# Kernel tuning notes

Hardware: AMD Instinct MI355X
Metric: run time of the kernel (lower is better)

Reference implementation:

```python
import jax, jax.numpy as jnp
import numpy as np

DIM = 1024
N_HEADS = 16
HEAD_DIM = DIM // N_HEADS
SCALE = HEAD_DIM ** -0.5


def setup_inputs() -> dict:
    key = jax.random.key(0)
    ks = jax.random.split(key, 5)
    B, N = 2, 2048
    x = jax.random.normal(ks[0], (B, N, DIM), dtype=jnp.float32)
    # torch Linear: y = x @ W.T + b, W shape (out, in)
    qkv_w = jax.random.normal(ks[1], (3 * DIM, DIM), dtype=jnp.float32) * (DIM ** -0.5)
    qkv_b = jax.random.normal(ks[2], (3 * DIM,), dtype=jnp.float32) * 0.02
    proj_w = jax.random.normal(ks[3], (DIM, DIM), dtype=jnp.float32) * (DIM ** -0.5)
    proj_b = jax.random.normal(ks[4], (DIM,), dtype=jnp.float32) * 0.02
    return {"x": x, "qkv_w": qkv_w, "qkv_b": qkv_b, "proj_w": proj_w, "proj_b": proj_b}


def reference(x, qkv_w, qkv_b, proj_w, proj_b):
    B, N, D = x.shape
    qkv = x @ qkv_w.T + qkv_b                      # [B, N, 3D]
    qkv = qkv.reshape(B, N, 3, N_HEADS, HEAD_DIM)
    qkv = jnp.transpose(qkv, (2, 0, 3, 1, 4))      # [3, B, H, N, hd]
    q, k, v = qkv[0], qkv[1], qkv[2]
    dp = jnp.einsum('bhqd,bhkd->bhqk', q, k) * SCALE  # [B, H, N, N]
    attn = jax.nn.softmax(dp, axis=-1)
    wa = jnp.einsum('bhqk,bhkd->bhqd', attn, v)    # [B, H, N, hd]
    wa = jnp.transpose(wa, (0, 2, 1, 3)).reshape(B, N, D)
    return wa @ proj_w.T + proj_b
```

## Files before the change

kernel.cpp:

```cpp
#include <hip/hip_runtime.h>

#define BATCH 2
#define SEQ   2048
#define DIM   1024
#define NHEAD 16
#define HD    64
#define BH    (BATCH * NHEAD)
#define SCALE 0.125f
#define LOG2E 1.44269504f
#define NTK   16

typedef __attribute__((ext_vector_type(8))) short short8;
typedef __attribute__((ext_vector_type(4))) short short4v;
typedef __attribute__((ext_vector_type(4))) float f32x4;
typedef __attribute__((ext_vector_type(16))) float f32x16;
typedef __attribute__((ext_vector_type(2))) unsigned int uint2v;

#define MFMA16(a, b, c) __builtin_amdgcn_mfma_f32_16x16x32_bf16(a, b, c, 0, 0, 0)
#define MFMA32(a, b, c) __builtin_amdgcn_mfma_f32_32x32x16_bf16(a, b, c, 0, 0, 0)

__device__ __forceinline__ ushort f2bf(float f) {
    union { float f; unsigned u; } v;
    v.f = f;
    unsigned r = (v.u + 0x7FFF + ((v.u >> 16) & 1)) >> 16;
    return (ushort)r;
}

__device__ __forceinline__ uint4 ld8f_bf16(const float* p) {
    float4 f0 = *(const float4*)p;
    float4 f1 = *(const float4*)(p + 4);
    union { ushort us[8]; uint4 v; } u;
    u.us[0] = f2bf(f0.x); u.us[1] = f2bf(f0.y);
    u.us[2] = f2bf(f0.z); u.us[3] = f2bf(f0.w);
    u.us[4] = f2bf(f1.x); u.us[5] = f2bf(f1.y);
    u.us[6] = f2bf(f1.z); u.us[7] = f2bf(f1.w);
    return u.v;
}

__device__ __forceinline__ void gl_lds16(const ushort* g, ushort* l) {
    __builtin_amdgcn_global_load_lds(
        (const __attribute__((address_space(1))) unsigned int*)g,
        (__attribute__((address_space(3))) unsigned int*)l,
        16, 0, 0);
}

__device__ __forceinline__ short8 ld_op(const ushort* base, int a1) {
    union { short4v h[2]; short8 v; } u;
    u.h[0] = *(const short4v*)&base[a1];
    u.h[1] = *(const short4v*)&base[a1 ^ 4];
    return u.v;
}

#define N_X  (BATCH * SEQ * DIM)
#define N_QW (3 * DIM * DIM)
#define N_PW (DIM * DIM)

__global__ __launch_bounds__(256) void cvt_kernel(
    const float* __restrict__ x, const float* __restrict__ qw,
    const float* __restrict__ pw, ushort* __restrict__ xb,
    ushort* __restrict__ qwb, ushort* __restrict__ pwb)
{
    const int i = (blockIdx.x * 256 + threadIdx.x) * 8;
    if (i < N_X)  *(uint4*)(xb  + i) = ld8f_bf16(x  + i);
    if (i < N_QW) *(uint4*)(qwb + i) = ld8f_bf16(qw + i);
    if (i < N_PW) *(uint4*)(pwb + i) = ld8f_bf16(pw + i);
}

template <int MODE, int WM, typename TOUT>
__global__ __launch_bounds__(256, 2) void gemm_bt(
    const ushort* __restrict__ A, const ushort* __restrict__ W,
    const float* __restrict__ bias, TOUT* __restrict__ out,
    int M, int Nout, int K)
{
    constexpr int BM = 2 * WM * 16;
    __shared__ __align__(16) ushort As[2][BM * 32];
    __shared__ __align__(16) ushort Bs[2][128 * 32];

    const int tid  = threadIdx.x;
    const int wave = tid >> 6, lane = tid & 63;
    const int quad = lane >> 4, l16 = lane & 15;
    const int wm = wave >> 1, wn = wave & 1;
    const int m0 = blockIdx.y * BM, n0 = blockIdx.x * 128;

    const int c0 = tid, c1 = tid + 256;
    const ushort* gA0 = A + (size_t)(m0 + (c0 >> 2)) * K + (c0 & 3) * 8;
    const ushort* gA1 = A + (size_t)(m0 + (c1 >> 2)) * K + (c1 & 3) * 8;
    const ushort* gB0 = W + (size_t)(n0 + (c0 >> 2)) * K + (c0 & 3) * 8;
    const ushort* gB1 = W + (size_t)(n0 + (c1 >> 2)) * K + (c1 & 3) * 8;

#define STAGE_G(buf, k0)                                                  \
    {                                                                     \
        gl_lds16(gA0 + (k0), &As[buf][(wave * 64) * 8]);                  \
        if (WM == 4) gl_lds16(gA1 + (k0), &As[buf][(wave * 64 + 256) * 8]); \
        gl_lds16(gB0 + (k0), &Bs[buf][(wave * 64) * 8]);                  \
        gl_lds16(gB1 + (k0), &Bs[buf][(wave * 64 + 256) * 8]);            \
    }

    f32x4 acc[WM][4];
#pragma unroll
    for (int i = 0; i < WM; i++)
#pragma unroll
        for (int j = 0; j < 4; j++) acc[i][j] = (f32x4){0.f, 0.f, 0.f, 0.f};

    const int KT = K >> 5;
    STAGE_G(0, 0)

    for (int kt = 0; kt < KT; kt++) {
        const int cur = kt & 1;
        __syncthreads();
        if (kt + 1 < KT) STAGE_G(cur ^ 1, (kt + 1) * 32)

        short8 af[WM], bfr[4];
#pragma unroll
        for (int mt = 0; mt < WM; mt++)
            af[mt] = *(const short8*)&As[cur][(wm * (WM * 16) + mt * 16 + l16) * 32 + quad * 8];
#pragma unroll
        for (int nt = 0; nt < 4; nt++)
            bfr[nt] = *(const short8*)&Bs[cur][(wn * 64 + nt * 16 + l16) * 32 + quad * 8];
#pragma unroll
        for (int mt = 0; mt < WM; mt++)
#pragma unroll
            for (int nt = 0; nt < 4; nt++)
                acc[mt][nt] = MFMA16(af[mt], bfr[nt], acc[mt][nt]);
    }

#pragma unroll
    for (int nt = 0; nt < 4; nt++) {
        const int n = n0 + wn * 64 + nt * 16 + l16;
        const float bv = bias[n];
#pragma unroll
        for (int mt = 0; mt < WM; mt++) {
            const int mBase = m0 + wm * (WM * 16) + mt * 16 + quad * 4;
#pragma unroll
            for (int r = 0; r < 4; r++) {
                const int m = mBase + r;
                float v = acc[mt][nt][r] + bv;
                if (MODE == 0) {
                    const int which = n >> 10, rem = n & 1023;
                    const int h = rem >> 6, d = rem & 63;
                    const int b = m >> 11, nq = m & 2047;
                    const int bh = b * NHEAD + h;
                    if (which == 0) v *= (SCALE * LOG2E);
                    size_t idx;
                    if (which == 2) {
                        const int nqs = (d & 1) ? (nq ^ 4) : nq;
                        idx = (size_t)2 * BH * SEQ * HD + ((size_t)bh * HD + d) * SEQ + nqs;
                    } else {
                        const int ds = (which == 1 && (nq & 1)) ? (d ^ 4) : d;
                        idx = (size_t)which * BH * SEQ * HD + ((size_t)bh * SEQ + nq) * HD + ds;
                    }
                    ((ushort*)out)[idx] = f2bf(v);
                } else {
                    ((float*)out)[(size_t)m * Nout + n] = v;
                }
            }
        }
    }
#undef STAGE_G
}

__global__ __launch_bounds__(512, 4) void attn_kernel(
    const ushort* __restrict__ qkv, ushort* __restrict__ wa)
{
    __shared__ __align__(16) ushort Ks[2][2][64 * 64];
    __shared__ __align__(16) ushort Vs[2][2][64 * 64];

    const int tid  = threadIdx.x;
    const int wave = tid >> 6, lane = tid & 63;
    const int l31  = lane & 31, hb = lane >> 5;
    const int h2 = wave >> 2, w4 = wave & 3;

    const int l = blockIdx.x;
    const int bh = (l & 7) + 8 * (l >> 7);
    const int qi = (l >> 3) & 15;
    const int b = bh >> 4, head = bh & 15;

    const size_t hOff = (size_t)bh * SEQ * HD;
    const ushort* Q  = qkv + hOff;
    const ushort* Kg = qkv + (size_t)BH * SEQ * HD + hOff;
    const ushort* Vt = qkv + (size_t)2 * BH * SEQ * HD + hOff;
    const int q0 = qi * 128 + w4 * 32;

    short8 qf[4];
#pragma unroll
    for (int i = 0; i < 4; i++)
        qf[i] = *(const short8*)&Q[(size_t)(q0 + l31) * HD + i * 16 + hb * 8];

    f32x16 o0, o1;
#pragma unroll
    for (int r = 0; r < 16; r++) { o0[r] = 0.f; o1[r] = 0.f; }
    f32x4 lacc = (f32x4){0.f, 0.f, 0.f, 0.f};

    const int rr = lane >> 3;
    const int cA = (((lane & 7) ^ (rr >> 1)) & 7) * 8;
    const ushort* KgA = Kg + rr * HD + cA;
    const ushort* KgB = Kg + rr * HD + (cA ^ 32);
    const ushort* VtA = Vt + (size_t)rr * SEQ + cA;
    const ushort* VtB = Vt + (size_t)rr * SEQ + (cA ^ 32);

#define STAGE(buf, kt)                                                          \
    {                                                                           \
        const size_t kO = (size_t)h2 * 1024 + (size_t)(kt) * 64;                \
        gl_lds16(KgA + (kO + w4 * 16    ) * HD, &Ks[h2][buf][(w4 * 16    ) * 64]); \
        gl_lds16(KgB + (kO + w4 * 16 + 8) * HD, &Ks[h2][buf][(w4 * 16 + 8) * 64]); \
        gl_lds16(VtA + (size_t)(w4 * 16    ) * SEQ + kO, &Vs[h2][buf][(w4 * 16    ) * 64]); \
        gl_lds16(VtB + (size_t)(w4 * 16 + 8) * SEQ + kO, &Vs[h2][buf][(w4 * 16 + 8) * 64]); \
    }

    STAGE(0, 0)

    const int sw2 = (l31 >> 1) & 7;
    const int pb  = (l31 & 1) * 4;

    for (int kt = 0; kt < NTK; kt++) {
        const int cur = kt & 1;
        __syncthreads();
        if (kt + 1 < NTK) STAGE(cur ^ 1, kt + 1)

        const ushort* kb_ = &Ks[h2][cur][0];
        const ushort* vb_ = &Vs[h2][cur][0];

        f32x16 z0, z1;
#pragma unroll
        for (int r = 0; r < 16; r++) { z0[r] = 0.f; z1[r] = 0.f; }

        __builtin_amdgcn_s_setprio(1);
#pragma unroll
        for (int i = 0; i < 4; i++) {
            const int co = (((2 * i + hb) ^ sw2) * 8) + pb;
            short8 ka0 = ld_op(kb_, (l31     ) * 64 + co);
            short8 ka1 = ld_op(kb_, (32 + l31) * 64 + co);
            z0 = MFMA32(ka0, qf[i], z0);
            z1 = MFMA32(ka1, qf[i], z1);
        }
        __builtin_amdgcn_s_setprio(0);

        unsigned u[2][8];
#pragma unroll
        for (int r = 0; r < 16; r++) {
            const float p0 = __builtin_amdgcn_exp2f(z0[r]);
            const float p1 = __builtin_amdgcn_exp2f(z1[r]);
            z0[r] = p0; z1[r] = p1;
            lacc[r & 3] += p0 + p1;
        }
#pragma unroll
        for (int m = 0; m < 8; m++) {
            unsigned pk;
            asm("v_cvt_pk_bf16_f32 %0, %1, %2"
                : "=v"(pk) : "v"(z0[2*m]), "v"(z0[2*m + 1]));
            u[0][m] = pk;
            asm("v_cvt_pk_bf16_f32 %0, %1, %2"
                : "=v"(pk) : "v"(z1[2*m]), "v"(z1[2*m + 1]));
            u[1][m] = pk;
        }

        __builtin_amdgcn_s_setprio(1);
#pragma unroll
        for (int i = 0; i < 4; i++) {
            const int kb = i >> 1, ii = i & 1;
            uint2v s0 = __builtin_amdgcn_permlane32_swap(
                u[kb][4*ii + 0], u[kb][4*ii + 2], false, false);
            uint2v s1 = __builtin_amdgcn_permlane32_swap(
                u[kb][4*ii + 1], u[kb][4*ii + 3], false, false);
            union { unsigned w[4]; short8 s; } pf;
            pf.w[0] = s0[0]; pf.w[1] = s1[0]; pf.w[2] = s0[1]; pf.w[3] = s1[1];
            const int co = (((2 * i + hb) ^ sw2) * 8) + pb;
            short8 vb0 = ld_op(vb_, (l31     ) * 64 + co);
            short8 vb1 = ld_op(vb_, (32 + l31) * 64 + co);
            o0 = MFMA32(pf.s, vb0, o0);
            o1 = MFMA32(pf.s, vb1, o1);
        }
        __builtin_amdgcn_s_setprio(0);
    }

    __syncthreads();

    float* Osc = (float*)&Ks[0][0][0];
    float* Lsc = (float*)&Vs[0][0][0];

    float lsum = lacc[0] + lacc[1] + lacc[2] + lacc[3];
    lsum += __shfl_xor(lsum, 32);
    if (lane < 32) Lsc[wave * 32 + l31] = lsum;

    if (h2 == 1) {
#pragma unroll
        for (int r = 0; r < 16; r++) {
            const int qr = (r & 3) + 8 * (r >> 2) + 4 * hb;
            Osc[w4 * 2048 + qr * 64 + l31]      = o0[r];
            Osc[w4 * 2048 + qr * 64 + 32 + l31] = o1[r];
        }
    }
    __syncthreads();

    if (h2 == 0) {
        const float inv = 1.f / (Lsc[w4 * 32 + l31] + Lsc[(4 + w4) * 32 + l31]);
#pragma unroll
        for (int r = 0; r < 16; r++) {
            const int qr = (r & 3) + 8 * (r >> 2) + 4 * hb;
            const float iv = __shfl(inv, qr);
            const float v0 = o0[r] + Osc[w4 * 2048 + qr * 64 + l31];
            const float v1 = o1[r] + Osc[w4 * 2048 + qr * 64 + 32 + l31];
            ushort* dst = wa + ((size_t)(b * SEQ + q0 + qr)) * DIM + head * HD + l31;
            dst[0]  = f2bf(v0 * iv);
            dst[32] = f2bf(v1 * iv);
        }
    }
#undef STAGE
}

extern "C" void kernel_launch(void* const* d_in, const int* in_sizes, int n_in,
                              void* d_out, int out_size, void* d_ws, size_t ws_size,
                              hipStream_t stream)
{
    const float* x      = (const float*)d_in[0];
    const float* qkv_w  = (const float*)d_in[1];
    const float* qkv_b  = (const float*)d_in[2];
    const float* proj_w = (const float*)d_in[3];
    const float* proj_b = (const float*)d_in[4];
    float* out = (float*)d_out;

    ushort* xb  = (ushort*)d_ws;
    ushort* qwb = xb  + (size_t)N_X;
    ushort* pwb = qwb + (size_t)N_QW;
    ushort* qkv = pwb + (size_t)N_PW;
    ushort* wa  = qkv + (size_t)3 * BH * SEQ * HD;

    const int M = BATCH * SEQ;
    dim3 blk(256);

    cvt_kernel<<<dim3((N_X / 8 + 255) / 256), blk, 0, stream>>>(
        x, qkv_w, proj_w, xb, qwb, pwb);

    gemm_bt<0, 4, ushort><<<dim3((3 * DIM) / 128, M / 128), blk, 0, stream>>>(
        xb, qwb, qkv_b, qkv, M, 3 * DIM, DIM);

    attn_kernel<<<dim3(512), dim3(512), 0, stream>>>(qkv, wa);

    gemm_bt<1, 2, float><<<dim3(DIM / 128, M / 64), blk, 0, stream>>>(
        wa, pwb, proj_b, out, M, DIM, DIM);
}
```

Before: 192.3 us.

## Remap GEMM workgroups across XCDs and move K/V swizzle from stores to loads

The GEMM kernels now use a 1D grid, and workgroup IDs are remapped so that consecutive tiles land on the same XCD (an 8-way interleave), which should improve L2 reuse of A/W tiles. The QKV GEMM also raises its min-waves launch bound from 2 to 3. The odd-row half swap for K and V is no longer applied when the GEMM epilogue scatters its writes. Instead, the attention kernel's LDS operand load selects which half comes first. That makes the global writes simpler, at the cost of a select per operand load in the inner loop.

```diff
diff --git a/kernel.cpp b/kernel.cpp
--- a/kernel.cpp
+++ b/kernel.cpp
@@ -44,10 +44,12 @@
         16, 0, 0);
 }
 
-__device__ __forceinline__ short8 ld_op(const ushort* base, int a1) {
+__device__ __forceinline__ short8 ld_op(const ushort* base, int a1, int odd) {
+    short4v x = *(const short4v*)&base[a1];
+    short4v y = *(const short4v*)&base[a1 ^ 4];
     union { short4v h[2]; short8 v; } u;
-    u.h[0] = *(const short4v*)&base[a1];
-    u.h[1] = *(const short4v*)&base[a1 ^ 4];
+    u.h[0] = odd ? y : x;
+    u.h[1] = odd ? x : y;
     return u.v;
 }
 
@@ -66,8 +68,8 @@
     if (i < N_PW) *(uint4*)(pwb + i) = ld8f_bf16(pw + i);
 }
 
-template <int MODE, int WM, typename TOUT>
-__global__ __launch_bounds__(256, 2) void gemm_bt(
+template <int MODE, int WM, int NBX, int MINW, typename TOUT>
+__global__ __launch_bounds__(256, MINW) void gemm_bt(
     const ushort* __restrict__ A, const ushort* __restrict__ W,
     const float* __restrict__ bias, TOUT* __restrict__ out,
     int M, int Nout, int K)
@@ -80,7 +82,11 @@
     const int wave = tid >> 6, lane = tid & 63;
     const int quad = lane >> 4, l16 = lane & 15;
     const int wm = wave >> 1, wn = wave & 1;
-    const int m0 = blockIdx.y * BM, n0 = blockIdx.x * 128;
+
+    const int wg  = blockIdx.x;
+    const int g8  = (int)gridDim.x >> 3;
+    const int lin = (wg & 7) * g8 + (wg >> 3);
+    const int m0 = (lin / NBX) * BM, n0 = (lin % NBX) * 128;
 
     const int c0 = tid, c1 = tid + 256;
     const ushort* gA0 = A + (size_t)(m0 + (c0 >> 2)) * K + (c0 & 3) * 8;
@@ -142,13 +148,10 @@
                     const int bh = b * NHEAD + h;
                     if (which == 0) v *= (SCALE * LOG2E);
                     size_t idx;
-                    if (which == 2) {
-                        const int nqs = (d & 1) ? (nq ^ 4) : nq;
-                        idx = (size_t)2 * BH * SEQ * HD + ((size_t)bh * HD + d) * SEQ + nqs;
-                    } else {
-                        const int ds = (which == 1 && (nq & 1)) ? (d ^ 4) : d;
-                        idx = (size_t)which * BH * SEQ * HD + ((size_t)bh * SEQ + nq) * HD + ds;
-                    }
+                    if (which == 2)
+                        idx = (size_t)2 * BH * SEQ * HD + ((size_t)bh * HD + d) * SEQ + nq;
+                    else
+                        idx = (size_t)which * BH * SEQ * HD + ((size_t)bh * SEQ + nq) * HD + d;
                     ((ushort*)out)[idx] = f2bf(v);
                 } else {
                     ((float*)out)[(size_t)m * Nout + n] = v;
@@ -228,8 +231,8 @@
 #pragma unroll
         for (int i = 0; i < 4; i++) {
             const int co = (((2 * i + hb) ^ sw2) * 8) + pb;
-            short8 ka0 = ld_op(kb_, (l31     ) * 64 + co);
-            short8 ka1 = ld_op(kb_, (32 + l31) * 64 + co);
+            short8 ka0 = ld_op(kb_, (l31     ) * 64 + co, pb);
+            short8 ka1 = ld_op(kb_, (32 + l31) * 64 + co, pb);
             z0 = MFMA32(ka0, qf[i], z0);
             z1 = MFMA32(ka1, qf[i], z1);
         }
@@ -265,8 +268,8 @@
             union { unsigned w[4]; short8 s; } pf;
             pf.w[0] = s0[0]; pf.w[1] = s1[0]; pf.w[2] = s0[1]; pf.w[3] = s1[1];
             const int co = (((2 * i + hb) ^ sw2) * 8) + pb;
-            short8 vb0 = ld_op(vb_, (l31     ) * 64 + co);
-            short8 vb1 = ld_op(vb_, (32 + l31) * 64 + co);
+            short8 vb0 = ld_op(vb_, (l31     ) * 64 + co, pb);
+            short8 vb1 = ld_op(vb_, (32 + l31) * 64 + co, pb);
             o0 = MFMA32(pf.s, vb0, o0);
             o1 = MFMA32(pf.s, vb1, o1);
         }
@@ -331,11 +334,11 @@
     cvt_kernel<<<dim3((N_X / 8 + 255) / 256), blk, 0, stream>>>(
         x, qkv_w, proj_w, xb, qwb, pwb);
 
-    gemm_bt<0, 4, ushort><<<dim3((3 * DIM) / 128, M / 128), blk, 0, stream>>>(
+    gemm_bt<0, 4, 24, 3, ushort><<<dim3(768), blk, 0, stream>>>(
         xb, qwb, qkv_b, qkv, M, 3 * DIM, DIM);
 
     attn_kernel<<<dim3(512), dim3(512), 0, stream>>>(qkv, wa);
 
-    gemm_bt<1, 2, float><<<dim3(DIM / 128, M / 64), blk, 0, stream>>>(
+    gemm_bt<1, 2, 8, 2, float><<<dim3(512), blk, 0, stream>>>(
         wa, pwb, proj_b, out, M, DIM, DIM);
 }
```

New measurement: 187.2 us. 1.03x faster.
